# Optimization experiments

Measured on AMD Instinct MI355X. Metric: run time of the kernel, lower is better.

The kernel has to match this reference:

```python
import jax, jax.numpy as jnp
import numpy as np

B, S, D = 2, 2048, 2048
H = 16
I = 8192  # intermediate_size
HD = I // H  # per-head intermediate dim = 512


def setup_inputs() -> dict:
    key = jax.random.key(0)
    ks = jax.random.split(key, 7)
    scale_d = 1.0 / np.sqrt(D)
    scale_i = 1.0 / np.sqrt(I)
    return {
        "x": jax.random.normal(ks[0], (B, S, D), dtype=jnp.float32),
        "adjacency": jax.random.uniform(ks[1], (B, H, S, S), dtype=jnp.float32) * (1.0 / S),
        "Wg": jax.random.normal(ks[2], (D, I), dtype=jnp.float32) * scale_d,
        "Wu": jax.random.normal(ks[3], (D, I), dtype=jnp.float32) * scale_d,
        "Wd": jax.random.normal(ks[4], (I, D), dtype=jnp.float32) * scale_i,
        "eps": jnp.zeros((H,), dtype=jnp.float32),
        "alpha": jnp.ones((H,), dtype=jnp.float32),
    }


def reference(x, adjacency, Wg, Wu, Wd, eps, alpha):
    # gate/up projections + SwiGLU: (B,S,I)
    gate = jnp.einsum("bsd,di->bsi", x, Wg)
    up = jnp.einsum("bsd,di->bsi", x, Wu)
    h_inter = jax.nn.silu(gate) * up
    # split into heads: (B,H,S,HD)
    h_heads = h_inter.reshape(B, S, H, HD).transpose(0, 2, 1, 3)
    # batched per-head GIN: (1+eps_h)*h + alpha_h * A_h @ h, all heads at once
    agg = jnp.einsum("bhst,bhtd->bhsd", adjacency, h_heads)
    e = (1.0 + eps)[None, :, None, None]
    a = alpha[None, :, None, None]
    h_gin = e * h_heads + a * agg
    # recombine heads -> (B,S,I), then down projection
    h_comb = h_gin.transpose(0, 2, 1, 3).reshape(B, S, I)
    return jnp.einsum("bsi,id->bsd", h_comb, Wd)
```

## Files before the change

kernel.cpp:

```cpp
#include <hip/hip_runtime.h>
#include <hip/hip_bf16.h>


typedef __bf16 bf16x8 __attribute__((ext_vector_type(8)));
typedef float f32x4 __attribute__((ext_vector_type(4)));

__device__ __forceinline__ unsigned short f2bf(float f) {
    union { float f; unsigned int u; } x; x.f = f;
    unsigned int r = x.u + 0x7fffu + ((x.u >> 16) & 1u);
    return (unsigned short)(r >> 16);
}
__device__ __forceinline__ float bf2f(unsigned short b) {
    union { unsigned int u; float f; } x; x.u = ((unsigned int)b) << 16;
    return x.f;
}

__device__ __forceinline__ void gload_lds16(const void* g, void* l) {
    __builtin_amdgcn_global_load_lds((const __attribute__((address_space(1))) void*)g,
                                     (__attribute__((address_space(3))) void*)l,
                                     16, 0, 0);
}


__global__ void conv_kernel(const float* __restrict__ in, unsigned short* __restrict__ out) {
    size_t i = ((size_t)blockIdx.x * 256 + threadIdx.x) * 4;
    float4 v = *(const float4*)(in + i);
    ushort4 o; o.x = f2bf(v.x); o.y = f2bf(v.y); o.z = f2bf(v.z); o.w = f2bf(v.w);
    *(ushort4*)(out + i) = o;
}

__global__ void tconv_kernel(const float* __restrict__ in, unsigned short* __restrict__ out,
                             int R, int C) {
    __shared__ float tile[64][65];
    int nbc = C >> 6;
    int bc = blockIdx.x % nbc, br = blockIdx.x / nbc;
    int r0 = br * 64, c0 = bc * 64;
    int t = threadIdx.x;
#pragma unroll
    for (int i = 0; i < 4; ++i) {
        int idx = i * 256 + t;
        int r = idx >> 4, c4 = (idx & 15) * 4;
        float4 v = *(const float4*)(in + (size_t)(r0 + r) * C + c0 + c4);
        tile[r][c4] = v.x; tile[r][c4 + 1] = v.y; tile[r][c4 + 2] = v.z; tile[r][c4 + 3] = v.w;
    }
    __syncthreads();
#pragma unroll
    for (int i = 0; i < 4; ++i) {
        int idx = i * 256 + t;
        int c = idx >> 4, r4 = (idx & 15) * 4;
        ushort4 o;
        o.x = f2bf(tile[r4][c]); o.y = f2bf(tile[r4 + 1][c]);
        o.z = f2bf(tile[r4 + 2][c]); o.w = f2bf(tile[r4 + 3][c]);
        *(ushort4*)(out + (size_t)(c0 + c) * R + r0 + r4) = o;
    }
}

template<int EPI>
__global__ void __launch_bounds__(512, 2) gemm256(
    const unsigned short* __restrict__ Ag,
    const unsigned short* __restrict__ Bg,
    const unsigned short* __restrict__ gbuf_c,
    unsigned short* __restrict__ gbuf,
    unsigned short* __restrict__ hhT)
{
    const int K = 2048;
    __shared__ unsigned short LDS[4][16384];
    int bid = (int)blockIdx.x;
    int lb = (bid & 7) * 64 + (bid >> 3);
    int nt = lb & 31, mt = lb >> 5;
    int tid = threadIdx.x, lane = tid & 63, wave = tid >> 6;
    int wm = wave >> 2, wn = wave & 3;
    int l15 = lane & 15, l4 = lane >> 4;

    f32x4 acc[8][4] = {};

    int jl = (lane & 7) ^ (lane >> 3);
    int prow0 = wave * 16 + (lane >> 3);
    int row0 = prow0 + ((jl & 4) << 5);
    int cc = (jl & 3) << 3;
    const unsigned short* srcA0 = Ag + (size_t)(mt * 256 + row0) * K + cc;
    const unsigned short* srcA1 = srcA0 + (size_t)8 * K;
    const unsigned short* srcB0 = Bg + (size_t)(nt * 256 + row0) * K + cc;
    const unsigned short* srcB1 = srcB0 + (size_t)8 * K;

    int cA = l15 * 128 + (((l4 + wm * 4) ^ (l15 & 7)) << 4);
    int cB = ((wn & 1) * 64 + l15) * 128 + (((l4 + ((wn >> 1) << 2)) ^ (l15 & 7)) << 4);

#define STAGE_A(t_) do { char* d_ = (char*)&LDS[(t_) & 3][0] + wave * 2048;              \
        gload_lds16((const void*)(srcA0 + (size_t)(t_) * 32), (void*)d_);                \
        gload_lds16((const void*)(srcA1 + (size_t)(t_) * 32), (void*)(d_ + 1024)); } while (0)
#define STAGE_B(t_) do { char* d_ = (char*)&LDS[(t_) & 3][8192] + wave * 2048;           \
        gload_lds16((const void*)(srcB0 + (size_t)(t_) * 32), (void*)d_);                \
        gload_lds16((const void*)(srcB1 + (size_t)(t_) * 32), (void*)(d_ + 1024)); } while (0)

    STAGE_A(0); STAGE_B(0);
    STAGE_A(1); STAGE_B(1);
    STAGE_A(2); STAGE_B(2);

    for (int t = 0; t < 64; ++t) {
        if (t + 2 < 64)      asm volatile("s_waitcnt vmcnt(8)" ::: "memory");
        else if (t + 1 < 64) asm volatile("s_waitcnt vmcnt(4)" ::: "memory");
        else                 asm volatile("s_waitcnt vmcnt(0)" ::: "memory");
        __builtin_amdgcn_s_barrier();
        const char* Abase = (const char*)&LDS[t & 3][0];
        const char* Bbase = Abase + 16384;
        bool more = (t + 3) < 64;
        if (more) STAGE_A(t + 3);
        bf16x8 bf[4], af[4];
#pragma unroll
        for (int ni = 0; ni < 4; ++ni) bf[ni] = *(const bf16x8*)(Bbase + cB + ni * 2048);
#pragma unroll
        for (int mi = 0; mi < 4; ++mi) af[mi] = *(const bf16x8*)(Abase + cA + mi * 2048);
        __builtin_amdgcn_s_setprio(1);
#pragma unroll
        for (int mi = 0; mi < 4; ++mi)
#pragma unroll
            for (int ni = 0; ni < 4; ++ni)
                acc[mi][ni] = __builtin_amdgcn_mfma_f32_16x16x32_bf16(af[mi], bf[ni], acc[mi][ni], 0, 0, 0);
        __builtin_amdgcn_s_setprio(0);
        if (more) STAGE_B(t + 3);
#pragma unroll
        for (int mi = 0; mi < 4; ++mi) af[mi] = *(const bf16x8*)(Abase + cA + 8192 + mi * 2048);
        __builtin_amdgcn_s_setprio(1);
#pragma unroll
        for (int mi = 0; mi < 4; ++mi)
#pragma unroll
            for (int ni = 0; ni < 4; ++ni)
                acc[4 + mi][ni] = __builtin_amdgcn_mfma_f32_16x16x32_bf16(af[mi], bf[ni], acc[4 + mi][ni], 0, 0, 0);
        __builtin_amdgcn_s_setprio(0);
    }
#undef STAGE_A
#undef STAGE_B

    if (EPI == 0) {
        ushort4* g4 = (ushort4*)gbuf;
        size_t base = ((size_t)lb * 32) * 512 + tid;
#pragma unroll
        for (int a = 0; a < 8; ++a)
#pragma unroll
            for (int ni = 0; ni < 4; ++ni) {
                f32x4 v = acc[a][ni];
                ushort4 o;
                o.x = f2bf(v[0]); o.y = f2bf(v[1]); o.z = f2bf(v[2]); o.w = f2bf(v[3]);
                g4[base + (size_t)(a * 4 + ni) * 512] = o;
            }
    } else {
        const ushort4* g4 = (const ushort4*)gbuf_c;
        size_t base = ((size_t)lb * 32) * 512 + tid;
        int rowb = mt * 256 + wm * 128 + l4 * 4;
        int colb = nt * 256 + wn * 64 + l15;
        int b = mt >> 3;
#pragma unroll
        for (int a = 0; a < 8; ++a)
#pragma unroll
            for (int ni = 0; ni < 4; ++ni) {
                ushort4 gq = g4[base + (size_t)(a * 4 + ni) * 512];
                int row = rowb + a * 16;
                int n = colb + ni * 16;
                ushort4 hv;
#pragma unroll
                for (int r = 0; r < 4; ++r) {
                    float gv = bf2f(((const unsigned short*)&gq)[r]);
                    float u = acc[a][ni][r];
                    float h = gv / (1.f + __expf(-gv)) * u;
                    ((unsigned short*)&hv)[r] = f2bf(h);
                }
                *(ushort4*)(hhT + ((size_t)b * 8192 + n) * 2048 + (row & 2047)) = hv;
            }
    }
}

__global__ void __launch_bounds__(512, 2) gemm_agg4(
    const float* __restrict__ adj,
    const unsigned short* __restrict__ hhT,
    const float* __restrict__ eps, const float* __restrict__ alpha,
    unsigned short* __restrict__ hcomb)
{
    const int S = 2048, HD = 512, I = 8192;
    __shared__ unsigned short As[2][128 * 40];
    __shared__ unsigned short Bs[4][512 * 32];
    int bid = (int)blockIdx.x;
    int lb = (bid & 7) * 64 + (bid >> 3);
    int pair = lb >> 4;
    int mt = lb & 15;
    int b = pair >> 4, h = pair & 15;
    int tid = threadIdx.x, lane = tid & 63, wave = tid >> 6;
    int wm = wave >> 2, wn = wave & 3;
    int l15 = lane & 15, l4 = lane >> 4;
    f32x4 acc[4][8] = {};

    float e1 = 1.f + eps[h];
    float a1 = alpha[h];
    bool a1z = (a1 == 0.f);
    float dfac = a1z ? 0.f : (e1 / a1);

    const float* Ab = adj + ((size_t)pair * S + (size_t)mt * 128) * S;
    const unsigned short* Bb = hhT + ((size_t)b * I + (size_t)h * HD) * (size_t)S;

    int a_row0 = tid >> 3, a_c = (tid & 7) << 2;
    int grow0 = mt * 128 + a_row0;

    int jl = (lane & 7) ^ (lane >> 3);
    int prow0 = wave * 16 + (lane >> 3);
    int browB = prow0 + ((jl & 4) << 6);
    int ccB = (jl & 3) << 3;
    const unsigned short* srcB = Bb + (size_t)browB * S + ccB;

#define BSTAGE(t_) do {                                                           \
        char* d_ = (char*)&Bs[(t_) & 3][0] + wave * 2048;                         \
        const unsigned short* s_ = srcB + (size_t)(t_) * 32;                      \
        gload_lds16((const void*)s_, (void*)d_);                                  \
        gload_lds16((const void*)(s_ + (size_t)8 * S), (void*)(d_ + 1024));       \
        gload_lds16((const void*)(s_ + (size_t)128 * S), (void*)(d_ + 16384));    \
        gload_lds16((const void*)(s_ + (size_t)136 * S), (void*)(d_ + 17408));    \
    } while (0)

    float4 pa0_0, pa1_0, pa0_1, pa1_1;

#define ALOAD(SET, K0)                                                            \
    do {                                                                          \
        pa0_##SET = *(const float4*)(Ab + (size_t)a_row0 * S + (K0) + a_c);       \
        pa1_##SET = *(const float4*)(Ab + (size_t)(a_row0 + 64) * S + (K0) + a_c);\
    } while (0)

#define ACONV(SET, BUF, K0)                                                       \
    do {                                                                          \
        int j0 = grow0 - (K0) - a_c;                                              \
        pa0_##SET.x += (j0 == 0) ? dfac : 0.f;                                    \
        pa0_##SET.y += (j0 == 1) ? dfac : 0.f;                                    \
        pa0_##SET.z += (j0 == 2) ? dfac : 0.f;                                    \
        pa0_##SET.w += (j0 == 3) ? dfac : 0.f;                                    \
        int j1 = j0 + 64;                                                         \
        pa1_##SET.x += (j1 == 0) ? dfac : 0.f;                                    \
        pa1_##SET.y += (j1 == 1) ? dfac : 0.f;                                    \
        pa1_##SET.z += (j1 == 2) ? dfac : 0.f;                                    \
        pa1_##SET.w += (j1 == 3) ? dfac : 0.f;                                    \
        ushort4 o0, o1;                                                           \
        o0.x = f2bf(pa0_##SET.x); o0.y = f2bf(pa0_##SET.y);                       \
        o0.z = f2bf(pa0_##SET.z); o0.w = f2bf(pa0_##SET.w);                       \
        o1.x = f2bf(pa1_##SET.x); o1.y = f2bf(pa1_##SET.y);                       \
        o1.z = f2bf(pa1_##SET.z); o1.w = f2bf(pa1_##SET.w);                       \
        *(ushort4*)((char*)As[BUF] + a_row0 * 80 + a_c * 2) = o0;                 \
        *(ushort4*)((char*)As[BUF] + (a_row0 + 64) * 80 + a_c * 2) = o1;          \
    } while (0)

    int koff2 = l4 << 4;
    const char* aptr0 = (const char*)As[0] + (wm * 64 + l15) * 80 + koff2;
    const char* aptr1 = (const char*)As[1] + (wm * 64 + l15) * 80 + koff2;
    int cB = ((wn & 1) * 128 + l15) * 128 + (((l4 + ((wn >> 1) << 2)) ^ (l15 & 7)) << 4);

#define AGG_COMPUTE(APTR, BBASE)                                                        \
    do {                                                                                \
        bf16x8 af[4], bfv[8];                                                           \
        _Pragma("unroll")                                                               \
        for (int mi = 0; mi < 4; ++mi) af[mi] = *(const bf16x8*)((APTR) + mi * 16 * 80);\
        _Pragma("unroll")                                                               \
        for (int ni = 0; ni < 8; ++ni) bfv[ni] = *(const bf16x8*)((BBASE) + cB + ni * 2048);\
        __builtin_amdgcn_s_setprio(1);                                                  \
        _Pragma("unroll")                                                               \
        for (int mi = 0; mi < 4; ++mi)                                                  \
            _Pragma("unroll")                                                           \
            for (int ni = 0; ni < 8; ++ni)                                              \
                acc[mi][ni] = __builtin_amdgcn_mfma_f32_16x16x32_bf16(af[mi], bfv[ni],  \
                                                                      acc[mi][ni], 0, 0, 0); \
        __builtin_amdgcn_s_setprio(0);                                                  \
    } while (0)

    BSTAGE(0);
    ALOAD(0, 0);
    BSTAGE(1);
    ALOAD(1, 32);
    BSTAGE(2);
    ACONV(0, 0, 0);
    asm volatile("s_waitcnt lgkmcnt(0)" ::: "memory");
    __builtin_amdgcn_s_barrier();

    for (int s = 0; s < 64; s += 2) {
        AGG_COMPUTE(aptr0, (const char*)&Bs[s & 3][0]);
        ACONV(1, 1, (s + 1) * 32);
        if (s + 2 < 64) ALOAD(0, (s + 2) * 32);
        if (s + 3 < 64) BSTAGE(s + 3);
        asm volatile("s_waitcnt lgkmcnt(0)" ::: "memory");
        __builtin_amdgcn_s_barrier();
        AGG_COMPUTE(aptr1, (const char*)&Bs[(s + 1) & 3][0]);
        if (s + 2 < 64) {
            ACONV(0, 0, (s + 2) * 32);
            if (s + 3 < 64) ALOAD(1, (s + 3) * 32);
            if (s + 4 < 64) BSTAGE(s + 4);
            asm volatile("s_waitcnt lgkmcnt(0)" ::: "memory");
            __builtin_amdgcn_s_barrier();
        }
    }
#undef BSTAGE
#undef ALOAD
#undef ACONV
#undef AGG_COMPUTE

    int s_base = mt * 128 + wm * 64;
    int d_base = wn * 128;
    if (!a1z) {
#pragma unroll
        for (int mi = 0; mi < 4; ++mi)
#pragma unroll
            for (int ni = 0; ni < 8; ++ni) {
                int sb = s_base + mi * 16 + ((lane >> 4) << 2);
                int d = d_base + ni * 16 + (lane & 15);
#pragma unroll
                for (int r = 0; r < 4; ++r) {
                    size_t off = ((size_t)(b * S + sb + r)) * I + (size_t)h * HD + d;
                    hcomb[off] = f2bf(a1 * acc[mi][ni][r]);
                }
            }
    } else {
#pragma unroll
        for (int mi = 0; mi < 4; ++mi)
#pragma unroll
            for (int ni = 0; ni < 8; ++ni) {
                int sb = s_base + mi * 16 + ((lane >> 4) << 2);
                int d = d_base + ni * 16 + (lane & 15);
                size_t col = (size_t)h * HD + d;
                ushort4 hq = *(const ushort4*)(hhT + ((size_t)b * I + col) * S + sb);
#pragma unroll
                for (int r = 0; r < 4; ++r) {
                    size_t off = ((size_t)(b * S + sb + r)) * I + col;
                    hcomb[off] = f2bf(e1 * bf2f(((const unsigned short*)&hq)[r]));
                }
            }
    }
}

__global__ void __launch_bounds__(512, 2) gemm_out2(
    const unsigned short* __restrict__ hcomb,
    const unsigned short* __restrict__ WdT,
    float* __restrict__ out)
{
    const int K = 8192;
    __shared__ unsigned short LDS[6][12288];
    int bid = (int)blockIdx.x;
    int lb = (bid & 7) * 32 + (bid >> 3);
    int mt = lb >> 4, nt = lb & 15;
    int tid = threadIdx.x, lane = tid & 63, wave = tid >> 6;
    int wm = wave >> 1, wn = wave & 1;
    int l15 = lane & 15, l4 = lane >> 4;
    f32x4 acc[4][4] = {};

    int jl = (lane & 7) ^ (lane >> 3);
    int prowA = wave * 16 + (lane >> 3);
    int rowA0 = prowA + ((jl & 4) << 5);
    int ccA = (jl & 3) << 3;
    const unsigned short* srcA0 = hcomb + (size_t)(mt * 256 + rowA0) * K + ccA;
    const unsigned short* srcA1 = srcA0 + (size_t)8 * K;
    int prowB = tid >> 3;
    int jbl = (tid & 7) ^ (prowB & 7);
    int rowB0 = prowB + ((jbl & 4) << 4);
    int ccB = (jbl & 3) << 3;
    const unsigned short* srcB0 = WdT + (size_t)(nt * 128 + rowB0) * K + ccB;

    int cA0 = ((wm & 1) * 64 + l15) * 128 + (((((wm >> 1) << 2) + l4) ^ (l15 & 7)) << 4);
    int cB0 = l15 * 128 + ((((wn << 2) + l4) ^ (l15 & 7)) << 4);

#define OSTAGE(t_) do {                                                                  \
        char* dA = (char*)&LDS[(t_) % 6][0] + wave * 2048;                               \
        gload_lds16((const void*)(srcA0 + (size_t)(t_) * 32), (void*)dA);                \
        gload_lds16((const void*)(srcA1 + (size_t)(t_) * 32), (void*)(dA + 1024));       \
        char* dB = (char*)&LDS[(t_) % 6][8192] + wave * 1024;                            \
        gload_lds16((const void*)(srcB0 + (size_t)(t_) * 32), (void*)dB);                \
    } while (0)

    OSTAGE(0); OSTAGE(1); OSTAGE(2); OSTAGE(3);

    for (int t = 0; t < 256; ++t) {
        if (t + 3 < 256)      asm volatile("s_waitcnt vmcnt(9)" ::: "memory");
        else if (t + 2 < 256) asm volatile("s_waitcnt vmcnt(6)" ::: "memory");
        else if (t + 1 < 256) asm volatile("s_waitcnt vmcnt(3)" ::: "memory");
        else                  asm volatile("s_waitcnt vmcnt(0)" ::: "memory");
        __builtin_amdgcn_s_barrier();
        const char* Abase = (const char*)&LDS[t % 6][0];
        const char* Bbase = Abase + 16384;
        bool more = (t + 4) < 256;
        bf16x8 af[4], bf[4];
#pragma unroll
        for (int ni = 0; ni < 4; ++ni) bf[ni] = *(const bf16x8*)(Bbase + cB0 + ni * 2048);
        if (more) OSTAGE(t + 4);
#pragma unroll
        for (int mi = 0; mi < 4; ++mi) af[mi] = *(const bf16x8*)(Abase + cA0 + mi * 2048);
        __builtin_amdgcn_s_setprio(1);
#pragma unroll
        for (int mi = 0; mi < 4; ++mi)
#pragma unroll
            for (int ni = 0; ni < 4; ++ni)
                acc[mi][ni] = __builtin_amdgcn_mfma_f32_16x16x32_bf16(af[mi], bf[ni], acc[mi][ni], 0, 0, 0);
        __builtin_amdgcn_s_setprio(0);
    }
#undef OSTAGE

    int m_off = mt * 256 + wm * 64, n_off = nt * 128 + wn * 64;
#pragma unroll
    for (int mi = 0; mi < 4; ++mi)
#pragma unroll
        for (int ni = 0; ni < 4; ++ni) {
            int mbase = m_off + mi * 16 + l4 * 4;
            int n = n_off + ni * 16 + l15;
#pragma unroll
            for (int r = 0; r < 4; ++r)
                out[(size_t)(mbase + r) * 2048 + n] = acc[mi][ni][r];
        }
}

extern "C" void kernel_launch(void* const* d_in, const int* in_sizes, int n_in,
                              void* d_out, int out_size, void* d_ws, size_t ws_size,
                              hipStream_t stream) {
    const float* x     = (const float*)d_in[0];
    const float* adj   = (const float*)d_in[1];
    const float* Wg    = (const float*)d_in[2];
    const float* Wu    = (const float*)d_in[3];
    const float* Wd    = (const float*)d_in[4];
    const float* eps   = (const float*)d_in[5];
    const float* alpha = (const float*)d_in[6];
    float* out = (float*)d_out;

    unsigned short* ws    = (unsigned short*)d_ws;
    unsigned short* xb    = ws;
    unsigned short* WgT   = xb + (size_t)4096 * 2048;
    unsigned short* WuT   = WgT + (size_t)8192 * 2048;
    unsigned short* WdT   = WuT + (size_t)8192 * 2048;
    unsigned short* hhT   = WdT + (size_t)2048 * 8192;
    unsigned short* hcomb = hhT + (size_t)16384 * 2048;
    unsigned short* gbuf  = hcomb;

    conv_kernel<<<8192, 256, 0, stream>>>(x, xb);
    tconv_kernel<<<4096, 256, 0, stream>>>(Wg, WgT, 2048, 8192);
    tconv_kernel<<<4096, 256, 0, stream>>>(Wu, WuT, 2048, 8192);
    tconv_kernel<<<4096, 256, 0, stream>>>(Wd, WdT, 8192, 2048);
    gemm256<0><<<512, 512, 0, stream>>>(xb, WgT, nullptr, gbuf, nullptr);
    gemm256<1><<<512, 512, 0, stream>>>(xb, WuT, gbuf, nullptr, hhT);
    gemm_agg4<<<512, 512, 0, stream>>>(adj, hhT, eps, alpha, hcomb);
    gemm_out2<<<256, 512, 0, stream>>>(hcomb, WdT, out);
}
```

Before: 719.5 us.

## Fuse gate and up projections into one GEMM with in-register SwiGLU epilogue

Replaces the two separate gate and up GEMM launches, which passed the gate result through a bf16 global buffer, with a single kernel. Each block computes a 256x128 tile of both gate and up, sharing the staged x tile, and applies SiLU(gate)*up directly from the accumulators. This removes the gbuf write and read round-trip and reloads x only once per output tile. In exchange the grid doubles to 1024 blocks of narrower N tiles, and the LDS B layout and wave mapping change.

```diff
diff --git a/kernel.cpp b/kernel.cpp
--- a/kernel.cpp
+++ b/kernel.cpp
@@ -55,47 +55,54 @@
     }
 }
 
-template<int EPI>
-__global__ void __launch_bounds__(512, 2) gemm256(
-    const unsigned short* __restrict__ Ag,
-    const unsigned short* __restrict__ Bg,
-    const unsigned short* __restrict__ gbuf_c,
-    unsigned short* __restrict__ gbuf,
+__global__ void __launch_bounds__(512, 2) gemm_gu(
+    const unsigned short* __restrict__ xb,
+    const unsigned short* __restrict__ WgT,
+    const unsigned short* __restrict__ WuT,
     unsigned short* __restrict__ hhT)
 {
     const int K = 2048;
     __shared__ unsigned short LDS[4][16384];
     int bid = (int)blockIdx.x;
-    int lb = (bid & 7) * 64 + (bid >> 3);
-    int nt = lb & 31, mt = lb >> 5;
+    int lb = (bid & 7) * 128 + (bid >> 3);
+    int mt = lb >> 6, nt = lb & 63;
     int tid = threadIdx.x, lane = tid & 63, wave = tid >> 6;
-    int wm = wave >> 2, wn = wave & 3;
+    int wm = wave >> 1, wn = wave & 1;
     int l15 = lane & 15, l4 = lane >> 4;
 
-    f32x4 acc[8][4] = {};
+    f32x4 accg[4][4] = {};
+    f32x4 accu[4][4] = {};
 
     int jl = (lane & 7) ^ (lane >> 3);
-    int prow0 = wave * 16 + (lane >> 3);
-    int row0 = prow0 + ((jl & 4) << 5);
-    int cc = (jl & 3) << 3;
-    const unsigned short* srcA0 = Ag + (size_t)(mt * 256 + row0) * K + cc;
+    int prowA = wave * 16 + (lane >> 3);
+    int rowA0 = prowA + ((jl & 4) << 5);
+    int ccA = (jl & 3) << 3;
+    const unsigned short* srcA0 = xb + (size_t)(mt * 256 + rowA0) * K + ccA;
     const unsigned short* srcA1 = srcA0 + (size_t)8 * K;
-    const unsigned short* srcB0 = Bg + (size_t)(nt * 256 + row0) * K + cc;
-    const unsigned short* srcB1 = srcB0 + (size_t)8 * K;
-
-    int cA = l15 * 128 + (((l4 + wm * 4) ^ (l15 & 7)) << 4);
-    int cB = ((wn & 1) * 64 + l15) * 128 + (((l4 + ((wn >> 1) << 2)) ^ (l15 & 7)) << 4);
-
-#define STAGE_A(t_) do { char* d_ = (char*)&LDS[(t_) & 3][0] + wave * 2048;              \
-        gload_lds16((const void*)(srcA0 + (size_t)(t_) * 32), (void*)d_);                \
-        gload_lds16((const void*)(srcA1 + (size_t)(t_) * 32), (void*)(d_ + 1024)); } while (0)
-#define STAGE_B(t_) do { char* d_ = (char*)&LDS[(t_) & 3][8192] + wave * 2048;           \
-        gload_lds16((const void*)(srcB0 + (size_t)(t_) * 32), (void*)d_);                \
-        gload_lds16((const void*)(srcB1 + (size_t)(t_) * 32), (void*)(d_ + 1024)); } while (0)
-
-    STAGE_A(0); STAGE_B(0);
-    STAGE_A(1); STAGE_B(1);
-    STAGE_A(2); STAGE_B(2);
+    int prowB = tid >> 3;
+    int jbl = (tid & 7) ^ (prowB & 7);
+    int rowB0 = prowB + ((jbl & 4) << 4);
+    int ccB = (jbl & 3) << 3;
+    const unsigned short* srcBg = WgT + (size_t)(nt * 128 + rowB0) * K + ccB;
+    const unsigned short* srcBu = WuT + (size_t)(nt * 128 + rowB0) * K + ccB;
+
+    int cA0 = ((wm & 1) * 64 + l15) * 128 + (((((wm >> 1) << 2) + l4) ^ (l15 & 7)) << 4);
+    int cB0 = l15 * 128 + ((((wn << 2) + l4) ^ (l15 & 7)) << 4);
+
+#define GU_STAGE_A(t_) do {                                                              \
+        char* dA = (char*)&LDS[(t_) & 3][0] + wave * 2048;                               \
+        gload_lds16((const void*)(srcA0 + (size_t)(t_) * 32), (void*)dA);                \
+        gload_lds16((const void*)(srcA1 + (size_t)(t_) * 32), (void*)(dA + 1024));       \
+    } while (0)
+#define GU_STAGE_B(t_) do {                                                              \
+        char* dB = (char*)&LDS[(t_) & 3][8192] + wave * 1024;                            \
+        gload_lds16((const void*)(srcBg + (size_t)(t_) * 32), (void*)dB);                \
+        gload_lds16((const void*)(srcBu + (size_t)(t_) * 32), (void*)(dB + 8192));       \
+    } while (0)
+
+    GU_STAGE_A(0); GU_STAGE_B(0);
+    GU_STAGE_A(1); GU_STAGE_B(1);
+    GU_STAGE_A(2); GU_STAGE_B(2);
 
     for (int t = 0; t < 64; ++t) {
         if (t + 2 < 64)      asm volatile("s_waitcnt vmcnt(8)" ::: "memory");
@@ -103,71 +110,53 @@
         else                 asm volatile("s_waitcnt vmcnt(0)" ::: "memory");
         __builtin_amdgcn_s_barrier();
         const char* Abase = (const char*)&LDS[t & 3][0];
-        const char* Bbase = Abase + 16384;
         bool more = (t + 3) < 64;
-        if (more) STAGE_A(t + 3);
-        bf16x8 bf[4], af[4];
-#pragma unroll
-        for (int ni = 0; ni < 4; ++ni) bf[ni] = *(const bf16x8*)(Bbase + cB + ni * 2048);
-#pragma unroll
-        for (int mi = 0; mi < 4; ++mi) af[mi] = *(const bf16x8*)(Abase + cA + mi * 2048);
+        if (more) GU_STAGE_A(t + 3);
+        bf16x8 af[4], bf[4];
+#pragma unroll
+        for (int ni = 0; ni < 4; ++ni) bf[ni] = *(const bf16x8*)(Abase + 16384 + cB0 + ni * 2048);
+#pragma unroll
+        for (int mi = 0; mi < 4; ++mi) af[mi] = *(const bf16x8*)(Abase + cA0 + mi * 2048);
         __builtin_amdgcn_s_setprio(1);
 #pragma unroll
         for (int mi = 0; mi < 4; ++mi)
 #pragma unroll
             for (int ni = 0; ni < 4; ++ni)
-                acc[mi][ni] = __builtin_amdgcn_mfma_f32_16x16x32_bf16(af[mi], bf[ni], acc[mi][ni], 0, 0, 0);
+                accg[mi][ni] = __builtin_amdgcn_mfma_f32_16x16x32_bf16(af[mi], bf[ni], accg[mi][ni], 0, 0, 0);
         __builtin_amdgcn_s_setprio(0);
-        if (more) STAGE_B(t + 3);
-#pragma unroll
-        for (int mi = 0; mi < 4; ++mi) af[mi] = *(const bf16x8*)(Abase + cA + 8192 + mi * 2048);
+        if (more) GU_STAGE_B(t + 3);
+#pragma unroll
+        for (int ni = 0; ni < 4; ++ni) bf[ni] = *(const bf16x8*)(Abase + 24576 + cB0 + ni * 2048);
         __builtin_amdgcn_s_setprio(1);
 #pragma unroll
         for (int mi = 0; mi < 4; ++mi)
 #pragma unroll
             for (int ni = 0; ni < 4; ++ni)
-                acc[4 + mi][ni] = __builtin_amdgcn_mfma_f32_16x16x32_bf16(af[mi], bf[ni], acc[4 + mi][ni], 0, 0, 0);
+                accu[mi][ni] = __builtin_amdgcn_mfma_f32_16x16x32_bf16(af[mi], bf[ni], accu[mi][ni], 0, 0, 0);
         __builtin_amdgcn_s_setprio(0);
     }
-#undef STAGE_A
-#undef STAGE_B
-
-    if (EPI == 0) {
-        ushort4* g4 = (ushort4*)gbuf;
-        size_t base = ((size_t)lb * 32) * 512 + tid;
-#pragma unroll
-        for (int a = 0; a < 8; ++a)
-#pragma unroll
-            for (int ni = 0; ni < 4; ++ni) {
-                f32x4 v = acc[a][ni];
-                ushort4 o;
-                o.x = f2bf(v[0]); o.y = f2bf(v[1]); o.z = f2bf(v[2]); o.w = f2bf(v[3]);
-                g4[base + (size_t)(a * 4 + ni) * 512] = o;
+#undef GU_STAGE_A
+#undef GU_STAGE_B
+
+    int rowb = mt * 256 + wm * 64 + l4 * 4;
+    int colb = nt * 128 + wn * 64 + l15;
+    int b = mt >> 3;
+#pragma unroll
+    for (int mi = 0; mi < 4; ++mi)
+#pragma unroll
+        for (int ni = 0; ni < 4; ++ni) {
+            int row = rowb + mi * 16;
+            int n = colb + ni * 16;
+            ushort4 hv;
+#pragma unroll
+            for (int r = 0; r < 4; ++r) {
+                float g = accg[mi][ni][r];
+                float u = accu[mi][ni][r];
+                float h = g / (1.f + __expf(-g)) * u;
+                ((unsigned short*)&hv)[r] = f2bf(h);
             }
-    } else {
-        const ushort4* g4 = (const ushort4*)gbuf_c;
-        size_t base = ((size_t)lb * 32) * 512 + tid;
-        int rowb = mt * 256 + wm * 128 + l4 * 4;
-        int colb = nt * 256 + wn * 64 + l15;
-        int b = mt >> 3;
-#pragma unroll
-        for (int a = 0; a < 8; ++a)
-#pragma unroll
-            for (int ni = 0; ni < 4; ++ni) {
-                ushort4 gq = g4[base + (size_t)(a * 4 + ni) * 512];
-                int row = rowb + a * 16;
-                int n = colb + ni * 16;
-                ushort4 hv;
-#pragma unroll
-                for (int r = 0; r < 4; ++r) {
-                    float gv = bf2f(((const unsigned short*)&gq)[r]);
-                    float u = acc[a][ni][r];
-                    float h = gv / (1.f + __expf(-gv)) * u;
-                    ((unsigned short*)&hv)[r] = f2bf(h);
-                }
-                *(ushort4*)(hhT + ((size_t)b * 8192 + n) * 2048 + (row & 2047)) = hv;
-            }
-    }
+            *(ushort4*)(hhT + ((size_t)b * 8192 + n) * 2048 + (row & 2047)) = hv;
+        }
 }
 
 __global__ void __launch_bounds__(512, 2) gemm_agg4(
@@ -426,14 +415,12 @@
     unsigned short* WdT   = WuT + (size_t)8192 * 2048;
     unsigned short* hhT   = WdT + (size_t)2048 * 8192;
     unsigned short* hcomb = hhT + (size_t)16384 * 2048;
-    unsigned short* gbuf  = hcomb;
 
     conv_kernel<<<8192, 256, 0, stream>>>(x, xb);
     tconv_kernel<<<4096, 256, 0, stream>>>(Wg, WgT, 2048, 8192);
     tconv_kernel<<<4096, 256, 0, stream>>>(Wu, WuT, 2048, 8192);
     tconv_kernel<<<4096, 256, 0, stream>>>(Wd, WdT, 8192, 2048);
-    gemm256<0><<<512, 512, 0, stream>>>(xb, WgT, nullptr, gbuf, nullptr);
-    gemm256<1><<<512, 512, 0, stream>>>(xb, WuT, gbuf, nullptr, hhT);
+    gemm_gu<<<1024, 512, 0, stream>>>(xb, WgT, WuT, hhT);
     gemm_agg4<<<512, 512, 0, stream>>>(adj, hhT, eps, alpha, hcomb);
     gemm_out2<<<256, 512, 0, stream>>>(hcomb, WdT, out);
 }
```

After: 695.0 us. 3.4% less time.
